# Kernel tuning notes

Hardware: AMD Instinct MI355X
Metric: run time of the kernel (lower is better)

## Reference

```python
import jax, jax.numpy as jnp
import numpy as np


def conv2d(x, w, b, pad=0, groups=1):
    y = jax.lax.conv_general_dilated(
        x, w, (1, 1), [(pad, pad), (pad, pad)],
        dimension_numbers=('NCHW', 'OIHW', 'NCHW'), feature_group_count=groups)
    return y + b[None, :, None, None]


def layernorm(x, w, b, eps=1e-5):
    # per-pixel LayerNorm over channel dim (matches to_3d -> nn.LayerNorm(dim) -> to_4d)
    mu = x.mean(1, keepdims=True)
    var = ((x - mu) ** 2).mean(1, keepdims=True)
    return (x - mu) * jax.lax.rsqrt(var + eps) * w[None, :, None, None] + b[None, :, None, None]


def setup_inputs():
    key = jax.random.key(0)
    ks = jax.random.split(key, 16)
    B, C, H, W = 1, 64, 64, 64
    heads, dh = 8, 8
    inner = heads * dh          # 64
    hid_lc = 32                 # max(16, inner // 2)
    hid_f = 4 * C               # 256, ffn_expansion_factor = 4
    def s(k, shape, fan):
        return (jax.random.normal(k, shape, jnp.float32) / np.float32(np.sqrt(fan)))
    return {
        'x': jax.random.normal(ks[0], (B, C, H, W), jnp.float32),
        'luma': jax.random.uniform(ks[1], (B, 1, H, W), jnp.float32),
        'ln1_w': jnp.ones((C,), jnp.float32), 'ln1_b': jnp.zeros((C,), jnp.float32),
        'qkv_w': s(ks[2], (3 * inner, C, 1, 1), C), 'qkv_b': jnp.zeros((3 * inner,), jnp.float32),
        'proj_w': s(ks[3], (C, inner, 1, 1), inner), 'proj_b': jnp.zeros((C,), jnp.float32),
        'lc1_w': s(ks[4], (hid_lc, 1, 3, 3), 9), 'lc1_b': jnp.zeros((hid_lc,), jnp.float32),
        'lc2_w': s(ks[5], (hid_lc, hid_lc, 3, 3), 9 * hid_lc), 'lc2_b': jnp.zeros((hid_lc,), jnp.float32),
        'gam_w': s(ks[6], (inner, hid_lc, 1, 1), hid_lc), 'gam_b': jnp.zeros((inner,), jnp.float32),
        'bet_w': s(ks[7], (inner, hid_lc, 1, 1), hid_lc), 'bet_b': jnp.zeros((inner,), jnp.float32),
        'alpha': jnp.float32(0.1),
        'ln2_w': jnp.ones((C,), jnp.float32), 'ln2_b': jnp.zeros((C,), jnp.float32),
        'ffn1_w': s(ks[8], (hid_f, C, 1, 1), C), 'ffn1_b': jnp.zeros((hid_f,), jnp.float32),
        'dw_w': s(ks[9], (hid_f, 1, 3, 3), 9), 'dw_b': jnp.zeros((hid_f,), jnp.float32),
        'ffn2_w': s(ks[10], (C, hid_f, 1, 1), hid_f), 'ffn2_b': jnp.zeros((C,), jnp.float32),
    }


def reference(x, luma, ln1_w, ln1_b, qkv_w, qkv_b, proj_w, proj_b,
              lc1_w, lc1_b, lc2_w, lc2_b, gam_w, gam_b, bet_w, bet_b, alpha,
              ln2_w, ln2_b, ffn1_w, ffn1_b, dw_w, dw_b, ffn2_w, ffn2_b):
    B, C, H, W = x.shape
    heads = 8
    N = H * W
    # --- attention branch ---
    xn = layernorm(x, ln1_w, ln1_b)
    qkv = conv2d(xn, qkv_w, qkv_b)             # [B, 3*inner, H, W]
    inner = qkv.shape[1] // 3
    dh = inner // heads

    def to_bhnd(t):  # b (h d) x y -> b h (x y) d
        return t.reshape(B, heads, dh, N).transpose(0, 1, 3, 2)

    q, k, v = [to_bhnd(t) for t in jnp.split(qkv, 3, axis=1)]
    # luma conditioning
    h1 = jax.nn.relu(conv2d(luma, lc1_w, lc1_b, pad=1))
    h1 = jax.nn.relu(conv2d(h1, lc2_w, lc2_b, pad=1))
    g = to_bhnd(conv2d(h1, gam_w, gam_b))
    bt = to_bhnd(conv2d(h1, bet_w, bet_b))
    q = g * q + bt
    k = g * k + bt
    v = g * v + bt
    # additive luma bias on q (avg_pool2d 3x3, count_include_pad=True -> fixed /9)
    invL = 1.0 - luma
    invL = jax.lax.reduce_window(invL, 0.0, jax.lax.add, (1, 1, 3, 3), (1, 1, 1, 1),
                                 [(0, 0), (0, 0), (1, 1), (1, 1)]) / 9.0
    invL = invL.reshape(B, N)
    invL = invL - invL.mean(-1, keepdims=True)
    q = q + alpha * invL[:, None, :, None]
    scale = dh ** -0.5
    attn = jax.nn.softmax(jnp.einsum('bhid,bhjd->bhij', q, k) * scale, axis=-1)
    out = jnp.einsum('bhij,bhjd->bhid', attn, v)
    out = out.transpose(0, 1, 3, 2).reshape(B, inner, H, W)
    x = x + conv2d(out, proj_w, proj_b)
    # --- ConvFFN branch ---
    y = layernorm(x, ln2_w, ln2_b)
    y = conv2d(y, ffn1_w, ffn1_b)
    y = conv2d(y, dw_w, dw_b, pad=1, groups=y.shape[1])
    y = jax.nn.gelu(y, approximate=False)
    y = conv2d(y, ffn2_w, ffn2_b)
    return x + y
```

## Files before the change

### kernel.cpp

```cpp
#include <hip/hip_runtime.h>
#include <math.h>

#define NPIX 4096
#define IMG 64

typedef __attribute__((ext_vector_type(8))) short bf16x8;
typedef __attribute__((ext_vector_type(4))) float floatx4;
typedef __attribute__((ext_vector_type(4))) unsigned int uintx4;

__device__ __forceinline__ unsigned int split_pack(float x) {
  unsigned int u = __float_as_uint(x);
  unsigned int hif = u & 0xffff0000u;
  float lof = x - __uint_as_float(hif);
  return (u >> 16) | (__float_as_uint(lof) & 0xffff0000u);
}

__device__ __forceinline__ unsigned int hi_pair(float a, float b) {
  return (__float_as_uint(a) >> 16) | (__float_as_uint(b) & 0xffff0000u);
}

__global__ __launch_bounds__(256) void lc12_kernel(
    const float* __restrict__ luma, const float* __restrict__ w1,
    const float* __restrict__ b1, const float* __restrict__ w2,
    const float* __restrict__ b2, const float* __restrict__ x,
    float* __restrict__ h2, float* __restrict__ pooled,
    float* __restrict__ bsums, float* __restrict__ mu1,
    float* __restrict__ rs1, unsigned short* __restrict__ cbuf) {
  __shared__ float lum[400];
  __shared__ float sw1[288];
  __shared__ float tin[32][324];
  __shared__ float swt[4][32][9];
  __shared__ float red[256];
  int tile = blockIdx.x, ocg = blockIdx.y;
  int ty0 = (tile >> 2) * 16, tx0 = (tile & 3) * 16;
  int tid = threadIdx.x;
  if (tile == 0 && ocg == 0 && tid < 16) cbuf[tid] = (tid < 8) ? 0x3F80 : 0;
  for (int idx = tid; idx < 400; idx += 256) {
    int py = idx / 20, px = idx - py * 20;
    int gy = ty0 + py - 2, gx = tx0 + px - 2;
    lum[idx] = (gy >= 0 && gy < IMG && gx >= 0 && gx < IMG)
                   ? luma[gy * IMG + gx]
                   : 0.f;
  }
  for (int idx = tid; idx < 288; idx += 256) sw1[idx] = w1[idx];
  for (int idx = tid; idx < 1152; idx += 256) {
    int o = idx / 288, r = idx - o * 288;
    swt[o][r / 9][r % 9] = w2[(ocg * 4 + o) * 288 + r];
  }
  __syncthreads();
  for (int idx = tid; idx < 32 * 324; idx += 256) {
    int ic = idx / 324, pos = idx - ic * 324;
    int py = pos / 18, px = pos - py * 18;
    int gy = ty0 + py - 1, gx = tx0 + px - 1;
    float v = 0.f;
    if (gy >= 0 && gy < IMG && gx >= 0 && gx < IMG) {
      float s = b1[ic];
      const float* wp = &sw1[ic * 9];
#pragma unroll
      for (int dy = 0; dy < 3; dy++)
#pragma unroll
        for (int dx = 0; dx < 3; dx++)
          s = fmaf(wp[dy * 3 + dx], lum[(py + dy) * 20 + px + dx], s);
      v = fmaxf(s, 0.f);
    }
    tin[ic][pos] = v;
  }
  __syncthreads();
  int ly = tid >> 4, lx = tid & 15;
  int p = (ty0 + ly) * IMG + tx0 + lx;
  float acc[4];
#pragma unroll
  for (int o = 0; o < 4; o++) acc[o] = b2[ocg * 4 + o];
  for (int ic = 0; ic < 32; ic++) {
    float v[9];
#pragma unroll
    for (int dy = 0; dy < 3; dy++)
#pragma unroll
      for (int dx = 0; dx < 3; dx++)
        v[dy * 3 + dx] = tin[ic][(ly + dy) * 18 + lx + dx];
#pragma unroll
    for (int o = 0; o < 4; o++)
#pragma unroll
      for (int t = 0; t < 9; t++) acc[o] = fmaf(swt[o][ic][t], v[t], acc[o]);
  }
#pragma unroll
  for (int o = 0; o < 4; o++)
    h2[(ocg * 4 + o) * NPIX + p] = fmaxf(acc[o], 0.f);
  if (ocg == 0) {
    int gy = ty0 + ly, gx = tx0 + lx;
    float sv = 0.f;
#pragma unroll
    for (int dy = 0; dy < 3; dy++)
#pragma unroll
      for (int dx = 0; dx < 3; dx++)
        sv += lum[(ly + dy + 1) * 20 + lx + dx + 1];
    float cy = 3.f - (gy == 0 ? 1.f : 0.f) - (gy == 63 ? 1.f : 0.f);
    float cx = 3.f - (gx == 0 ? 1.f : 0.f) - (gx == 63 ? 1.f : 0.f);
    float pv = (cy * cx - sv) * (1.f / 9.f);
    pooled[p] = pv;
    red[tid] = pv;
    __syncthreads();
    for (int st = 128; st > 0; st >>= 1) {
      if (tid < st) red[tid] += red[tid + st];
      __syncthreads();
    }
    if (tid == 0) bsums[tile] = red[0];
    float s = 0.f, q = 0.f;
#pragma unroll 8
    for (int cc = 0; cc < 64; cc++) {
      float xv = x[cc * NPIX + p];
      s += xv;
      q = fmaf(xv, xv, q);
    }
    float mu = s * (1.f / 64.f);
    mu1[p] = mu;
    rs1[p] = rsqrtf(q * (1.f / 64.f) - mu * mu + 1e-5f);
  }
}

__global__ __launch_bounds__(256) void ln_qkv_kernel(
    const float* __restrict__ X, const float* __restrict__ mu1,
    const float* __restrict__ rs1, const float* __restrict__ lnw,
    const float* __restrict__ lnb, const float* __restrict__ W,
    const float* __restrict__ bias, const float* __restrict__ gamW,
    const float* __restrict__ gamB, const float* __restrict__ betW,
    const float* __restrict__ betB, const float* __restrict__ h2,
    const float* __restrict__ pooled, const float* __restrict__ bsums,
    const float* __restrict__ alpha, unsigned short* __restrict__ qhl,
    unsigned short* __restrict__ khl, unsigned short* __restrict__ vthx,
    unsigned short* __restrict__ vtlx) {
  const float QSCALE = 0.35355339059327376f * 1.4426950408889634f;
  __shared__ float xs[64][32];
  __shared__ float wsh[64][64];
  __shared__ float h2s[32][32];
  __shared__ float wgs[32][64];
  __shared__ float wbs[32][64];
  __shared__ float mu[32];
  __shared__ float rs[32];
  int n0 = blockIdx.x * 32, part = blockIdx.y, m0 = part * 64;
  int tid = threadIdx.x;
  if (tid < 32) {
    mu[tid] = mu1[n0 + tid];
    rs[tid] = rs1[n0 + tid];
  }
  {
    int e = tid * 2;
    int c = e >> 3, off = (e & 7) * 4;
    *(float4*)&xs[c][off] = *(const float4*)&X[c * NPIX + n0 + off];
    int e1 = e + 1;
    int c1 = e1 >> 3, off1 = (e1 & 7) * 4;
    *(float4*)&xs[c1][off1] = *(const float4*)&X[c1 * NPIX + n0 + off1];
  }
  {
    int m = tid >> 2, kg = (tid & 3) * 16;
    const float4* wr = (const float4*)&W[(m0 + m) * 64 + kg];
    float4 w0 = wr[0], w1 = wr[1], w2 = wr[2], w3 = wr[3];
    float wv[16] = {w0.x, w0.y, w0.z, w0.w, w1.x, w1.y, w1.z, w1.w,
                    w2.x, w2.y, w2.z, w2.w, w3.x, w3.y, w3.z, w3.w};
#pragma unroll
    for (int j = 0; j < 16; j++) wsh[kg + j][m] = wv[j];
  }
  {
    int k = tid >> 3, nf = (tid & 7) * 4;
    *(float4*)&h2s[k][nf] = *(const float4*)&h2[k * NPIX + n0 + nf];
  }
  {
    int m = tid >> 2, kg = (tid & 3) * 8;
    const float4* g0 = (const float4*)&gamW[m * 32 + kg];
    float4 a = g0[0], b4 = g0[1];
    float gv[8] = {a.x, a.y, a.z, a.w, b4.x, b4.y, b4.z, b4.w};
#pragma unroll
    for (int j = 0; j < 8; j++) wgs[kg + j][m] = gv[j];
    const float4* bb0 = (const float4*)&betW[m * 32 + kg];
    float4 c4 = bb0[0], d4 = bb0[1];
    float bv[8] = {c4.x, c4.y, c4.z, c4.w, d4.x, d4.y, d4.z, d4.w};
#pragma unroll
    for (int j = 0; j < 8; j++) wbs[kg + j][m] = bv[j];
  }
  __syncthreads();
  {
    int c = tid >> 2, pg = (tid & 3) * 8;
    float wc = lnw[c], bc = lnb[c];
#pragma unroll
    for (int j = 0; j < 8; j++) {
      int p = pg + j;
      xs[c][p] = (xs[c][p] - mu[p]) * rs[p] * wc + bc;
    }
  }
  __syncthreads();
  int tx = tid & 15, ty = tid >> 4;
  float ga[4][2] = {}, ba[4][2] = {};
#pragma unroll 8
  for (int kk = 0; kk < 32; kk++) {
    float4 wg4 = *(const float4*)&wgs[kk][ty * 4];
    float4 wb4 = *(const float4*)&wbs[kk][ty * 4];
    float2 h22 = *(const float2*)&h2s[kk][tx * 2];
    float gv[4] = {wg4.x, wg4.y, wg4.z, wg4.w};
    float bv[4] = {wb4.x, wb4.y, wb4.z, wb4.w};
    float hv[2] = {h22.x, h22.y};
#pragma unroll
    for (int im = 0; im < 4; im++)
#pragma unroll
      for (int in = 0; in < 2; in++) {
        ga[im][in] = fmaf(gv[im], hv[in], ga[im][in]);
        ba[im][in] = fmaf(bv[im], hv[in], ba[im][in]);
      }
  }
#pragma unroll
  for (int im = 0; im < 4; im++) {
    int cc = ty * 4 + im;
    float gb = gamB[cc], bb2 = betB[cc];
#pragma unroll
    for (int in = 0; in < 2; in++) {
      ga[im][in] += gb;
      ba[im][in] += bb2;
    }
  }
  float acc[4][2] = {};
#pragma unroll 8
  for (int kk = 0; kk < 64; kk++) {
    float4 a = *(const float4*)&wsh[kk][ty * 4];
    float2 b2 = *(const float2*)&xs[kk][tx * 2];
    float av[4] = {a.x, a.y, a.z, a.w};
    float bv[2] = {b2.x, b2.y};
#pragma unroll
    for (int im = 0; im < 4; im++)
#pragma unroll
      for (int in = 0; in < 2; in++)
        acc[im][in] = fmaf(av[im], bv[in], acc[im][in]);
  }
  float val[4][2];
#pragma unroll
  for (int im = 0; im < 4; im++) {
    int cc = ty * 4 + im;
    float bv = bias[m0 + cc];
#pragma unroll
    for (int in = 0; in < 2; in++)
      val[im][in] = fmaf(ga[im][in], acc[im][in] + bv, ba[im][in]);
  }
  if (part == 0) {
    float msum = 0.f;
#pragma unroll
    for (int t = 0; t < 16; t++) msum += bsums[t];
    float mean = msum * (1.f / 4096.f);
    float a0 = alpha[0];
    const float2 pv = *(const float2*)&pooled[n0 + tx * 2];
    float iv[2] = {a0 * (pv.x - mean), a0 * (pv.y - mean)};
#pragma unroll
    for (int im = 0; im < 4; im++)
#pragma unroll
      for (int in = 0; in < 2; in++)
        val[im][in] = (val[im][in] + iv[in]) * QSCALE;
  }
  if (part < 2) {
    unsigned short* dst = (part == 0) ? qhl : khl;
    int h = ty >> 1, d0 = (ty & 1) * 4;
#pragma unroll
    for (int in = 0; in < 2; in++) {
      int n = n0 + tx * 2 + in;
      unsigned int pk[4];
#pragma unroll
      for (int im = 0; im < 4; im++) pk[im] = split_pack(val[im][in]);
      short4 hi, lo;
      hi.x = (short)(pk[0] & 0xffffu); hi.y = (short)(pk[1] & 0xffffu);
      hi.z = (short)(pk[2] & 0xffffu); hi.w = (short)(pk[3] & 0xffffu);
      lo.x = (short)(pk[0] >> 16); lo.y = (short)(pk[1] >> 16);
      lo.z = (short)(pk[2] >> 16); lo.w = (short)(pk[3] >> 16);
      unsigned short* base = dst + ((size_t)(h * NPIX + n) << 4) + d0;
      *(short4*)base = hi;
      *(short4*)(base + 8) = lo;
    }
  } else {
    int nq = n0 + tx * 2;
    int off0 = (nq >> 5) * 32 + ((nq >> 4) & 1) * 4 + ((nq >> 2) & 3) * 8 +
               (nq & 3);
#pragma unroll
    for (int im = 0; im < 4; im++) {
      int cc = ty * 4 + im;
      unsigned int pk0 = split_pack(val[im][0]);
      unsigned int pk1 = split_pack(val[im][1]);
      short2 hi, lo;
      hi.x = (short)(pk0 & 0xffffu);
      hi.y = (short)(pk1 & 0xffffu);
      lo.x = (short)(pk0 >> 16);
      lo.y = (short)(pk1 >> 16);
      *(short2*)(vthx + (size_t)cc * NPIX + off0) = hi;
      *(short2*)(vtlx + (size_t)cc * NPIX + off0) = lo;
    }
  }
}

__global__ __launch_bounds__(256, 4) void attn_kernel(
    const unsigned short* __restrict__ qhl,
    const unsigned short* __restrict__ khl,
    const unsigned short* __restrict__ vthx,
    const unsigned short* __restrict__ vtlx,
    const unsigned short* __restrict__ cbuf, float* __restrict__ pacc,
    float* __restrict__ pl) {
  int tid = threadIdx.x;
  int wave = tid >> 6, lane = tid & 63;
  int g = lane >> 4, c = lane & 15;
  int h = blockIdx.y, jp = blockIdx.z;
  int i0 = blockIdx.x * 256 + wave * 64;
  int jbase = jp * 512;
  bf16x8 qB[4];
#pragma unroll
  for (int t = 0; t < 4; t++)
    qB[t] = *(const bf16x8*)(qhl + ((size_t)(h * NPIX + i0 + t * 16 + c) << 4) +
                             ((g & 1) << 3));
  const unsigned short* kp =
      khl + ((size_t)(h * NPIX + jbase + c) << 4) + ((g >> 1) << 3);
  const unsigned short* vhp;
  const unsigned short* vlp;
  int vstep;
  if (c < 8) {
    vhp = vthx + (size_t)(h * 8 + c) * NPIX + jbase + (g << 3);
    vlp = vtlx + (size_t)(h * 8 + c) * NPIX + jbase + (g << 3);
    vstep = 32;
  } else {
    vhp = (c == 8) ? cbuf : (cbuf + 8);
    vlp = cbuf + 8;
    vstep = 0;
  }
  floatx4 zero4 = {0.f, 0.f, 0.f, 0.f};
  floatx4 aH[4], aM[4];
#pragma unroll
  for (int t = 0; t < 4; t++) {
    aH[t] = zero4;
    aM[t] = zero4;
  }
#pragma unroll 4
  for (int jt = 0; jt < 16; ++jt) {
    bf16x8 ka0 = *(const bf16x8*)kp;
    bf16x8 ka1 = *(const bf16x8*)(kp + 256);
    bf16x8 avh = *(const bf16x8*)vhp;
    bf16x8 avl = *(const bf16x8*)vlp;
    kp += 512;
    vhp += vstep;
    vlp += vstep;
#pragma unroll
    for (int t = 0; t < 4; t++) {
      floatx4 s0 =
          __builtin_amdgcn_mfma_f32_16x16x32_bf16(ka0, qB[t], zero4, 0, 0, 0);
      floatx4 s1 =
          __builtin_amdgcn_mfma_f32_16x16x32_bf16(ka1, qB[t], zero4, 0, 0, 0);
      float p0 = __builtin_amdgcn_exp2f(fminf(s0[0], 80.f));
      float p1 = __builtin_amdgcn_exp2f(fminf(s0[1], 80.f));
      float p2 = __builtin_amdgcn_exp2f(fminf(s0[2], 80.f));
      float p3 = __builtin_amdgcn_exp2f(fminf(s0[3], 80.f));
      float p4 = __builtin_amdgcn_exp2f(fminf(s1[0], 80.f));
      float p5 = __builtin_amdgcn_exp2f(fminf(s1[1], 80.f));
      float p6 = __builtin_amdgcn_exp2f(fminf(s1[2], 80.f));
      float p7 = __builtin_amdgcn_exp2f(fminf(s1[3], 80.f));
      uintx4 bh;
      bh.x = hi_pair(p0, p1);
      bh.y = hi_pair(p2, p3);
      bh.z = hi_pair(p4, p5);
      bh.w = hi_pair(p6, p7);
      bf16x8 pbh = __builtin_bit_cast(bf16x8, bh);
      aH[t] = __builtin_amdgcn_mfma_f32_16x16x32_bf16(avh, pbh, aH[t], 0, 0, 0);
      aM[t] = __builtin_amdgcn_mfma_f32_16x16x32_bf16(avl, pbh, aM[t], 0, 0, 0);
    }
  }
#pragma unroll
  for (int t = 0; t < 4; t++) {
    floatx4 o = aH[t] + aM[t];
    if (g < 2) {
      size_t b0 = (size_t)((jp * 8 + h) * NPIX + i0 + t * 16 + c);
      *(float4*)&pacc[b0 * 8 + g * 4] = make_float4(o[0], o[1], o[2], o[3]);
    } else if (g == 2) {
      pl[(size_t)((jp * 8 + h) * NPIX + i0 + t * 16 + c)] = o[0];
    }
  }
}

__global__ __launch_bounds__(256) void proj_ffn1_kernel(
    const float* __restrict__ pacc, const float* __restrict__ pl,
    const float* __restrict__ Wp, const float* __restrict__ bp,
    const float* __restrict__ x, const float* __restrict__ ln2w,
    const float* __restrict__ ln2b, const float* __restrict__ W1,
    const float* __restrict__ b1f, float* __restrict__ x1,
    float* __restrict__ f1) {
  __shared__ float at[64][33];
  __shared__ float wsh[64][64];
  __shared__ float w1s[64][64];
  __shared__ float xsl[64][33];
  __shared__ float ps[8][33];
  __shared__ float pq[8][33];
  __shared__ float mus[32];
  __shared__ float rss[32];
  int n0 = blockIdx.x * 32;
  int ch = blockIdx.y;
  int tid = threadIdx.x;
  {
    int mm = tid >> 2, kg = (tid & 3) * 16;
    const float4* wr = (const float4*)&Wp[mm * 64 + kg];
    float4 w0 = wr[0], w1 = wr[1], w2 = wr[2], w3 = wr[3];
    float wv[16] = {w0.x, w0.y, w0.z, w0.w, w1.x, w1.y, w1.z, w1.w,
                    w2.x, w2.y, w2.z, w2.w, w3.x, w3.y, w3.z, w3.w};
#pragma unroll
    for (int j = 0; j < 16; j++) wsh[kg + j][mm] = wv[j];
    const float4* w1r = (const float4*)&W1[(ch * 64 + mm) * 64 + kg];
    float4 u0 = w1r[0], u1 = w1r[1], u2 = w1r[2], u3 = w1r[3];
    float uv[16] = {u0.x, u0.y, u0.z, u0.w, u1.x, u1.y, u1.z, u1.w,
                    u2.x, u2.y, u2.z, u2.w, u3.x, u3.y, u3.z, u3.w};
#pragma unroll
    for (int j = 0; j < 16; j++) w1s[kg + j][mm] = uv[j];
  }
  {
    int hh = tid >> 5, nn = tid & 31;
    int i = n0 + nn;
    float L = 0.f, o[8] = {};
#pragma unroll
    for (int p = 0; p < 8; p++) {
      size_t base = (size_t)((p * 8 + hh) * NPIX + i);
      L += pl[base];
      const float4 a0 = *(const float4*)&pacc[base * 8];
      const float4 a1 = *(const float4*)&pacc[base * 8 + 4];
      o[0] += a0.x; o[1] += a0.y; o[2] += a0.z; o[3] += a0.w;
      o[4] += a1.x; o[5] += a1.y; o[6] += a1.z; o[7] += a1.w;
    }
    float inv = 1.f / L;
#pragma unroll
    for (int d = 0; d < 8; d++) at[hh * 8 + d][nn] = o[d] * inv;
  }
  __syncthreads();
  int ty = tid >> 5, tx = tid & 31;
  float acc[8] = {};
#pragma unroll 8
  for (int k = 0; k < 64; k++) {
    float b = at[k][tx];
    float4 a0 = *(const float4*)&wsh[k][ty * 8];
    float4 a1 = *(const float4*)&wsh[k][ty * 8 + 4];
    acc[0] = fmaf(a0.x, b, acc[0]);
    acc[1] = fmaf(a0.y, b, acc[1]);
    acc[2] = fmaf(a0.z, b, acc[2]);
    acc[3] = fmaf(a0.w, b, acc[3]);
    acc[4] = fmaf(a1.x, b, acc[4]);
    acc[5] = fmaf(a1.y, b, acc[5]);
    acc[6] = fmaf(a1.z, b, acc[6]);
    acc[7] = fmaf(a1.w, b, acc[7]);
  }
  float v[8], sn = 0.f, qn = 0.f;
#pragma unroll
  for (int im = 0; im < 8; im++) {
    int row = ty * 8 + im;
    float vv = acc[im] + bp[row] + x[row * NPIX + n0 + tx];
    v[im] = vv;
    sn += vv;
    qn = fmaf(vv, vv, qn);
  }
  if (ch == 0) {
#pragma unroll
    for (int im = 0; im < 8; im++)
      x1[(ty * 8 + im) * NPIX + n0 + tx] = v[im];
  }
  ps[ty][tx] = sn;
  pq[ty][tx] = qn;
  __syncthreads();
  if (tid < 32) {
    float s = 0.f, q = 0.f;
#pragma unroll
    for (int t = 0; t < 8; t++) {
      s += ps[t][tid];
      q += pq[t][tid];
    }
    float mu = s * (1.f / 64.f);
    mus[tid] = mu;
    rss[tid] = rsqrtf(q * (1.f / 64.f) - mu * mu + 1e-5f);
  }
  __syncthreads();
  {
    float muv = mus[tx], rsv = rss[tx];
#pragma unroll
    for (int im = 0; im < 8; im++) {
      int row = ty * 8 + im;
      xsl[row][tx] = (v[im] - muv) * rsv * ln2w[row] + ln2b[row];
    }
  }
  __syncthreads();
  float a2[8] = {};
#pragma unroll 8
  for (int k = 0; k < 64; k++) {
    float b = xsl[k][tx];
    float4 a0 = *(const float4*)&w1s[k][ty * 8];
    float4 a1 = *(const float4*)&w1s[k][ty * 8 + 4];
    a2[0] = fmaf(a0.x, b, a2[0]);
    a2[1] = fmaf(a0.y, b, a2[1]);
    a2[2] = fmaf(a0.z, b, a2[2]);
    a2[3] = fmaf(a0.w, b, a2[3]);
    a2[4] = fmaf(a1.x, b, a2[4]);
    a2[5] = fmaf(a1.y, b, a2[5]);
    a2[6] = fmaf(a1.z, b, a2[6]);
    a2[7] = fmaf(a1.w, b, a2[7]);
  }
#pragma unroll
  for (int im = 0; im < 8; im++) {
    int row = ch * 64 + ty * 8 + im;
    f1[row * NPIX + n0 + tx] = a2[im] + b1f[row];
  }
}

__global__ __launch_bounds__(256) void ffn2_dw_kernel(
    const float* __restrict__ f1, const float* __restrict__ dww,
    const float* __restrict__ dwb, const float* __restrict__ W,
    const float* __restrict__ bias, const float* __restrict__ resid,
    float* __restrict__ C) {
  __shared__ float xs[256][20];
  __shared__ float wsh[256][33];
  int n0 = blockIdx.x * 16, m0 = blockIdx.y * 32;
  int tid = threadIdx.x;
  int y = n0 >> 6, x0 = n0 & 63;
#pragma unroll
  for (int e = tid; e < 8192; e += 256) {
    int mm = e >> 8, kk = e & 255;
    wsh[kk][mm] = W[(m0 + mm) * 256 + kk];
  }
  {
    int px4 = (tid & 3) * 4;
    int xabs = x0 + px4;
#pragma unroll
    for (int k = 0; k < 4; k++) {
      int c = (tid >> 2) + 64 * k;
      const float* base = f1 + c * NPIX;
      float wv[9];
#pragma unroll
      for (int i = 0; i < 9; i++) wv[i] = dww[c * 9 + i];
      float bc = dwb[c];
      float a[4] = {bc, bc, bc, bc};
#pragma unroll
      for (int dy = 0; dy < 3; dy++) {
        int yy = y + dy - 1;
        if (yy < 0 || yy > 63) continue;
        const float* row = base + yy * IMG + xabs;
        float4 mid = *(const float4*)row;
        float left = (xabs > 0) ? row[-1] : 0.f;
        float right = (xabs + 4 < IMG) ? row[4] : 0.f;
        float win[6] = {left, mid.x, mid.y, mid.z, mid.w, right};
#pragma unroll
        for (int o = 0; o < 4; o++)
#pragma unroll
          for (int dx = 0; dx < 3; dx++)
            a[o] = fmaf(wv[dy * 3 + dx], win[o + dx], a[o]);
      }
      float4 o4;
      float* op = &o4.x;
#pragma unroll
      for (int o = 0; o < 4; o++)
        op[o] = 0.5f * a[o] * (1.f + erff(a[o] * 0.70710678118654752f));
      *(float4*)&xs[c][px4] = o4;
    }
  }
  __syncthreads();
  int m = tid >> 3, np = (tid & 7) * 2;
  float a0 = 0.f, a1 = 0.f;
#pragma unroll 8
  for (int kk = 0; kk < 256; kk++) {
    float w0 = wsh[kk][m];
    float b0 = xs[kk][np];
    float b1 = xs[kk][np + 1];
    a0 = fmaf(w0, b0, a0);
    a1 = fmaf(w0, b1, a1);
  }
  int row = m0 + m;
  float bv = bias[row];
  const float2 rr = *(const float2*)&resid[row * NPIX + n0 + np];
  *(float2*)&C[row * NPIX + n0 + np] =
      make_float2(a0 + bv + rr.x, a1 + bv + rr.y);
}

extern "C" void kernel_launch(void* const* d_in, const int* in_sizes, int n_in,
                              void* d_out, int out_size, void* d_ws,
                              size_t ws_size, hipStream_t stream) {
  const float* x      = (const float*)d_in[0];
  const float* luma   = (const float*)d_in[1];
  const float* ln1_w  = (const float*)d_in[2];
  const float* ln1_b  = (const float*)d_in[3];
  const float* qkv_w  = (const float*)d_in[4];
  const float* qkv_b  = (const float*)d_in[5];
  const float* proj_w = (const float*)d_in[6];
  const float* proj_b = (const float*)d_in[7];
  const float* lc1_w  = (const float*)d_in[8];
  const float* lc1_b  = (const float*)d_in[9];
  const float* lc2_w  = (const float*)d_in[10];
  const float* lc2_b  = (const float*)d_in[11];
  const float* gam_w  = (const float*)d_in[12];
  const float* gam_b  = (const float*)d_in[13];
  const float* bet_w  = (const float*)d_in[14];
  const float* bet_b  = (const float*)d_in[15];
  const float* alpha  = (const float*)d_in[16];
  const float* ln2_w  = (const float*)d_in[17];
  const float* ln2_b  = (const float*)d_in[18];
  const float* ffn1_w = (const float*)d_in[19];
  const float* ffn1_b = (const float*)d_in[20];
  const float* dw_w   = (const float*)d_in[21];
  const float* dw_b   = (const float*)d_in[22];
  const float* ffn2_w = (const float*)d_in[23];
  const float* ffn2_b = (const float*)d_in[24];
  float* out = (float*)d_out;

  float* w = (float*)d_ws;
  float* pooled = w + 0;
  float* bsums  = w + 4096;
  unsigned short* cbuf = (unsigned short*)(w + 4160);
  float* mu1 = w + 4224;
  float* rs1 = w + 8320;
  unsigned short* qhl  = (unsigned short*)(w + 12416);
  unsigned short* khl  = (unsigned short*)(w + 274560);
  unsigned short* vthx = (unsigned short*)(w + 536704);
  unsigned short* vtlx = (unsigned short*)(w + 667776);
  float* pacc = w + 798848;
  float* pl   = w + 2896000;
  float* x1   = w + 3158144;
  float* f1   = w + 3420288;
  float* h2   = w + 4468864;

  lc12_kernel<<<dim3(16, 8), 256, 0, stream>>>(luma, lc1_w, lc1_b, lc2_w,
                                               lc2_b, x, h2, pooled, bsums,
                                               mu1, rs1, cbuf);
  ln_qkv_kernel<<<dim3(128, 3), 256, 0, stream>>>(
      x, mu1, rs1, ln1_w, ln1_b, qkv_w, qkv_b, gam_w, gam_b, bet_w, bet_b, h2,
      pooled, bsums, alpha, qhl, khl, vthx, vtlx);
  attn_kernel<<<dim3(16, 8, 8), 256, 0, stream>>>(qhl, khl, vthx, vtlx, cbuf,
                                                  pacc, pl);
  proj_ffn1_kernel<<<dim3(128, 4), 256, 0, stream>>>(
      pacc, pl, proj_w, proj_b, x, ln2_w, ln2_b, ffn1_w, ffn1_b, x1, f1);
  ffn2_dw_kernel<<<dim3(256, 2), 256, 0, stream>>>(f1, dw_w, dw_b, ffn2_w,
                                                   ffn2_b, x1, out);
}
```

Before: 191.2 us.

## Retile proj/FFN1 and FFN2 GEMMs with vectorized LDS layouts and perm-based bf16 packing

Replaces the two-op bf16 high-half pack in the attention loop with a single byte-permute instruction. Retiles the proj/FFN1 kernel so each thread computes a 4x2 output block with float4/float2 LDS reads and float2 global stores, with padded shared arrays and a 16-row partial-sum reduction. Transposes the FFN2 shared layouts (K-contiguous weights and activations) so the inner loop uses float4 LDS reads, and loads weights with coalesced float4 copies. The aim is fewer LDS instructions and bank conflicts, at the cost of strided scalar LDS writes for the GELU output and changed register use.

```diff
diff --git a/kernel.cpp b/kernel.cpp
--- a/kernel.cpp
+++ b/kernel.cpp
@@ -15,8 +15,9 @@
   return (u >> 16) | (__float_as_uint(lof) & 0xffff0000u);
 }
 
-__device__ __forceinline__ unsigned int hi_pair(float a, float b) {
-  return (__float_as_uint(a) >> 16) | (__float_as_uint(b) & 0xffff0000u);
+__device__ __forceinline__ unsigned int pack_hi2(float a, float b) {
+  return __builtin_amdgcn_perm(__float_as_uint(b), __float_as_uint(a),
+                               0x07060302u);
 }
 
 __global__ __launch_bounds__(256) void lc12_kernel(
@@ -353,10 +354,10 @@
       float p6 = __builtin_amdgcn_exp2f(fminf(s1[2], 80.f));
       float p7 = __builtin_amdgcn_exp2f(fminf(s1[3], 80.f));
       uintx4 bh;
-      bh.x = hi_pair(p0, p1);
-      bh.y = hi_pair(p2, p3);
-      bh.z = hi_pair(p4, p5);
-      bh.w = hi_pair(p6, p7);
+      bh.x = pack_hi2(p0, p1);
+      bh.y = pack_hi2(p2, p3);
+      bh.z = pack_hi2(p4, p5);
+      bh.w = pack_hi2(p6, p7);
       bf16x8 pbh = __builtin_bit_cast(bf16x8, bh);
       aH[t] = __builtin_amdgcn_mfma_f32_16x16x32_bf16(avh, pbh, aH[t], 0, 0, 0);
       aM[t] = __builtin_amdgcn_mfma_f32_16x16x32_bf16(avl, pbh, aM[t], 0, 0, 0);
@@ -381,12 +382,12 @@
     const float* __restrict__ ln2b, const float* __restrict__ W1,
     const float* __restrict__ b1f, float* __restrict__ x1,
     float* __restrict__ f1) {
-  __shared__ float at[64][33];
-  __shared__ float wsh[64][64];
-  __shared__ float w1s[64][64];
-  __shared__ float xsl[64][33];
-  __shared__ float ps[8][33];
-  __shared__ float pq[8][33];
+  __shared__ float at[64][34];
+  __shared__ float wsh[64][68];
+  __shared__ float w1s[64][68];
+  __shared__ float xsl[64][34];
+  __shared__ float ps[16][34];
+  __shared__ float pq[16][34];
   __shared__ float mus[32];
   __shared__ float rss[32];
   int n0 = blockIdx.x * 32;
@@ -425,43 +426,51 @@
     for (int d = 0; d < 8; d++) at[hh * 8 + d][nn] = o[d] * inv;
   }
   __syncthreads();
-  int ty = tid >> 5, tx = tid & 31;
-  float acc[8] = {};
+  int mq = tid >> 4, pp = (tid & 15) * 2;
+  float acc[4][2] = {};
 #pragma unroll 8
   for (int k = 0; k < 64; k++) {
-    float b = at[k][tx];
-    float4 a0 = *(const float4*)&wsh[k][ty * 8];
-    float4 a1 = *(const float4*)&wsh[k][ty * 8 + 4];
-    acc[0] = fmaf(a0.x, b, acc[0]);
-    acc[1] = fmaf(a0.y, b, acc[1]);
-    acc[2] = fmaf(a0.z, b, acc[2]);
-    acc[3] = fmaf(a0.w, b, acc[3]);
-    acc[4] = fmaf(a1.x, b, acc[4]);
-    acc[5] = fmaf(a1.y, b, acc[5]);
-    acc[6] = fmaf(a1.z, b, acc[6]);
-    acc[7] = fmaf(a1.w, b, acc[7]);
-  }
-  float v[8], sn = 0.f, qn = 0.f;
-#pragma unroll
-  for (int im = 0; im < 8; im++) {
-    int row = ty * 8 + im;
-    float vv = acc[im] + bp[row] + x[row * NPIX + n0 + tx];
-    v[im] = vv;
-    sn += vv;
-    qn = fmaf(vv, vv, qn);
+    float4 w4 = *(const float4*)&wsh[k][mq * 4];
+    float2 b2 = *(const float2*)&at[k][pp];
+    acc[0][0] = fmaf(w4.x, b2.x, acc[0][0]);
+    acc[0][1] = fmaf(w4.x, b2.y, acc[0][1]);
+    acc[1][0] = fmaf(w4.y, b2.x, acc[1][0]);
+    acc[1][1] = fmaf(w4.y, b2.y, acc[1][1]);
+    acc[2][0] = fmaf(w4.z, b2.x, acc[2][0]);
+    acc[2][1] = fmaf(w4.z, b2.y, acc[2][1]);
+    acc[3][0] = fmaf(w4.w, b2.x, acc[3][0]);
+    acc[3][1] = fmaf(w4.w, b2.y, acc[3][1]);
+  }
+  float v[4][2], sn0 = 0.f, sn1 = 0.f, qn0 = 0.f, qn1 = 0.f;
+#pragma unroll
+  for (int im = 0; im < 4; im++) {
+    int row = mq * 4 + im;
+    float bpv = bp[row];
+    const float2 xr = *(const float2*)&x[row * NPIX + n0 + pp];
+    float v0 = acc[im][0] + bpv + xr.x;
+    float v1 = acc[im][1] + bpv + xr.y;
+    v[im][0] = v0;
+    v[im][1] = v1;
+    sn0 += v0;
+    qn0 = fmaf(v0, v0, qn0);
+    sn1 += v1;
+    qn1 = fmaf(v1, v1, qn1);
   }
   if (ch == 0) {
 #pragma unroll
-    for (int im = 0; im < 8; im++)
-      x1[(ty * 8 + im) * NPIX + n0 + tx] = v[im];
-  }
-  ps[ty][tx] = sn;
-  pq[ty][tx] = qn;
+    for (int im = 0; im < 4; im++)
+      *(float2*)&x1[(mq * 4 + im) * NPIX + n0 + pp] =
+          make_float2(v[im][0], v[im][1]);
+  }
+  ps[mq][pp] = sn0;
+  ps[mq][pp + 1] = sn1;
+  pq[mq][pp] = qn0;
+  pq[mq][pp + 1] = qn1;
   __syncthreads();
   if (tid < 32) {
     float s = 0.f, q = 0.f;
 #pragma unroll
-    for (int t = 0; t < 8; t++) {
+    for (int t = 0; t < 16; t++) {
       s += ps[t][tid];
       q += pq[t][tid];
     }
@@ -471,33 +480,38 @@
   }
   __syncthreads();
   {
-    float muv = mus[tx], rsv = rss[tx];
-#pragma unroll
-    for (int im = 0; im < 8; im++) {
-      int row = ty * 8 + im;
-      xsl[row][tx] = (v[im] - muv) * rsv * ln2w[row] + ln2b[row];
-    }
-  }
-  __syncthreads();
-  float a2[8] = {};
+    float mu0 = mus[pp], mu1v = mus[pp + 1];
+    float rs0 = rss[pp], rs1v = rss[pp + 1];
+#pragma unroll
+    for (int im = 0; im < 4; im++) {
+      int row = mq * 4 + im;
+      float w2v = ln2w[row], b2v = ln2b[row];
+      *(float2*)&xsl[row][pp] =
+          make_float2((v[im][0] - mu0) * rs0 * w2v + b2v,
+                      (v[im][1] - mu1v) * rs1v * w2v + b2v);
+    }
+  }
+  __syncthreads();
+  float a2[4][2] = {};
 #pragma unroll 8
   for (int k = 0; k < 64; k++) {
-    float b = xsl[k][tx];
-    float4 a0 = *(const float4*)&w1s[k][ty * 8];
-    float4 a1 = *(const float4*)&w1s[k][ty * 8 + 4];
-    a2[0] = fmaf(a0.x, b, a2[0]);
-    a2[1] = fmaf(a0.y, b, a2[1]);
-    a2[2] = fmaf(a0.z, b, a2[2]);
-    a2[3] = fmaf(a0.w, b, a2[3]);
-    a2[4] = fmaf(a1.x, b, a2[4]);
-    a2[5] = fmaf(a1.y, b, a2[5]);
-    a2[6] = fmaf(a1.z, b, a2[6]);
-    a2[7] = fmaf(a1.w, b, a2[7]);
-  }
-#pragma unroll
-  for (int im = 0; im < 8; im++) {
-    int row = ch * 64 + ty * 8 + im;
-    f1[row * NPIX + n0 + tx] = a2[im] + b1f[row];
+    float4 w4 = *(const float4*)&w1s[k][mq * 4];
+    float2 b2 = *(const float2*)&xsl[k][pp];
+    a2[0][0] = fmaf(w4.x, b2.x, a2[0][0]);
+    a2[0][1] = fmaf(w4.x, b2.y, a2[0][1]);
+    a2[1][0] = fmaf(w4.y, b2.x, a2[1][0]);
+    a2[1][1] = fmaf(w4.y, b2.y, a2[1][1]);
+    a2[2][0] = fmaf(w4.z, b2.x, a2[2][0]);
+    a2[2][1] = fmaf(w4.z, b2.y, a2[2][1]);
+    a2[3][0] = fmaf(w4.w, b2.x, a2[3][0]);
+    a2[3][1] = fmaf(w4.w, b2.y, a2[3][1]);
+  }
+#pragma unroll
+  for (int im = 0; im < 4; im++) {
+    int row = ch * 64 + mq * 4 + im;
+    float bb = b1f[row];
+    *(float2*)&f1[row * NPIX + n0 + pp] =
+        make_float2(a2[im][0] + bb, a2[im][1] + bb);
   }
 }
 
@@ -506,15 +520,17 @@
     const float* __restrict__ dwb, const float* __restrict__ W,
     const float* __restrict__ bias, const float* __restrict__ resid,
     float* __restrict__ C) {
-  __shared__ float xs[256][20];
-  __shared__ float wsh[256][33];
+  __shared__ float xs2[16][260];
+  __shared__ float wshT[32][260];
   int n0 = blockIdx.x * 16, m0 = blockIdx.y * 32;
   int tid = threadIdx.x;
   int y = n0 >> 6, x0 = n0 & 63;
-#pragma unroll
-  for (int e = tid; e < 8192; e += 256) {
-    int mm = e >> 8, kk = e & 255;
-    wsh[kk][mm] = W[(m0 + mm) * 256 + kk];
+  {
+    int mm = tid >> 3, kg = (tid & 7) * 32;
+    const float4* src = (const float4*)&W[(m0 + mm) * 256 + kg];
+    float4* dst = (float4*)&wshT[mm][kg];
+#pragma unroll
+    for (int i = 0; i < 8; i++) dst[i] = src[i];
   }
   {
     int px4 = (tid & 3) * 4;
@@ -543,24 +559,28 @@
           for (int dx = 0; dx < 3; dx++)
             a[o] = fmaf(wv[dy * 3 + dx], win[o + dx], a[o]);
       }
-      float4 o4;
-      float* op = &o4.x;
 #pragma unroll
       for (int o = 0; o < 4; o++)
-        op[o] = 0.5f * a[o] * (1.f + erff(a[o] * 0.70710678118654752f));
-      *(float4*)&xs[c][px4] = o4;
+        xs2[px4 + o][c] =
+            0.5f * a[o] * (1.f + erff(a[o] * 0.70710678118654752f));
     }
   }
   __syncthreads();
   int m = tid >> 3, np = (tid & 7) * 2;
   float a0 = 0.f, a1 = 0.f;
-#pragma unroll 8
-  for (int kk = 0; kk < 256; kk++) {
-    float w0 = wsh[kk][m];
-    float b0 = xs[kk][np];
-    float b1 = xs[kk][np + 1];
-    a0 = fmaf(w0, b0, a0);
-    a1 = fmaf(w0, b1, a1);
+#pragma unroll 4
+  for (int k4 = 0; k4 < 64; k4++) {
+    float4 w4 = *(const float4*)&wshT[m][k4 * 4];
+    float4 xa = *(const float4*)&xs2[np][k4 * 4];
+    float4 xb = *(const float4*)&xs2[np + 1][k4 * 4];
+    a0 = fmaf(w4.x, xa.x, a0);
+    a1 = fmaf(w4.x, xb.x, a1);
+    a0 = fmaf(w4.y, xa.y, a0);
+    a1 = fmaf(w4.y, xb.y, a1);
+    a0 = fmaf(w4.z, xa.z, a0);
+    a1 = fmaf(w4.z, xb.z, a1);
+    a0 = fmaf(w4.w, xa.w, a0);
+    a1 = fmaf(w4.w, xb.w, a1);
   }
   int row = m0 + m;
   float bv = bias[row];
```

After: 190.7 us. Within noise of the previous version (-0.2%).
